# Kernel tuning notes

Hardware: AMD Instinct MI355X
Metric: run time of the kernel (lower is better)

The kernel has to match this reference:

```python
import jax, jax.numpy as jnp
import numpy as np

COST_CLASS, COST_BBOX, COST_GIOU = 1.0, 5.0, 2.0


def _cxcywh_to_xyxy(b):
    cx, cy, w, h = b[..., 0], b[..., 1], b[..., 2], b[..., 3]
    return jnp.stack([cx - 0.5 * w, cy - 0.5 * h, cx + 0.5 * w, cy + 0.5 * h], axis=-1)


def _generalized_box_iou(boxes1, boxes2):
    # boxes1 [N,4], boxes2 [M,4] in xyxy -> [N,M] GIoU
    area1 = (boxes1[:, 2] - boxes1[:, 0]) * (boxes1[:, 3] - boxes1[:, 1])
    area2 = (boxes2[:, 2] - boxes2[:, 0]) * (boxes2[:, 3] - boxes2[:, 1])
    lt = jnp.maximum(boxes1[:, None, :2], boxes2[None, :, :2])
    rb = jnp.minimum(boxes1[:, None, 2:], boxes2[None, :, 2:])
    wh = jnp.clip(rb - lt, 0.0)
    inter = wh[..., 0] * wh[..., 1]
    union = area1[:, None] + area2[None, :] - inter
    iou = inter / union
    lt_e = jnp.minimum(boxes1[:, None, :2], boxes2[None, :, :2])
    rb_e = jnp.maximum(boxes1[:, None, 2:], boxes2[None, :, 2:])
    wh_e = jnp.clip(rb_e - lt_e, 0.0)
    area_e = wh_e[..., 0] * wh_e[..., 1]
    return iou - (area_e - union) / area_e


def setup_inputs() -> dict:
    key = jax.random.key(0)
    k1, k2, k3, k4 = jax.random.split(key, 4)
    B, Q, NC, T = 16, 900, 92, 1600
    return {
        "class_logits": jax.random.normal(k1, (B, Q, NC), dtype=jnp.float32),
        "box_regression": jax.random.uniform(k2, (B, Q, 4), dtype=jnp.float32),
        "tgt_ids": jax.random.randint(k3, (T,), 0, NC, dtype=jnp.int64),
        "tgt_bbox": jax.random.uniform(k4, (T, 4), dtype=jnp.float32),
    }


def reference(class_logits, box_regression, tgt_ids, tgt_bbox):
    B, Q, NC = class_logits.shape
    out_prob = jax.nn.softmax(class_logits.reshape(B * Q, NC), axis=-1)  # [BQ, NC]
    out_bbox = box_regression.reshape(B * Q, 4)                          # [BQ, 4]
    cost_class = -out_prob[:, tgt_ids]                                   # [BQ, T]
    cost_bbox = jnp.sum(jnp.abs(out_bbox[:, None, :] - tgt_bbox[None, :, :]), axis=-1)  # L1 cdist
    cost_giou = -_generalized_box_iou(_cxcywh_to_xyxy(out_bbox), _cxcywh_to_xyxy(tgt_bbox))
    C = COST_BBOX * cost_bbox + COST_CLASS * cost_class + COST_GIOU * cost_giou
    return C.reshape(B, Q, -1)
```

## Files before the change

kernel.cpp:

```cpp
#include <hip/hip_runtime.h>
#include <math.h>

#define BB 16
#define QQ 900
#define NC 92
#define NCP 96
#define TT 1600
#define BQ (BB * QQ)

#define RT 2
#define RTILE 8
#define NK 25

__global__ __launch_bounds__(256)
void k_cost(const float* __restrict__ logits,
            const float* __restrict__ boxes,
            const int* __restrict__ tids,
            const float* __restrict__ tbox,
            float* __restrict__ out) {
    __shared__ float pexp[RTILE][NCP];

    const int row0 = blockIdx.x * RTILE;

    {
        int idx = threadIdx.x * 2;
        int r = idx / NCP, c = idx - r * NCP;
        float2 v = make_float2(0.0f, 0.0f);
        if (c < NC) {
            float2 lv = *(const float2*)&logits[(row0 + r) * NC + c];
            v.x = __expf(lv.x); v.y = __expf(lv.y);
        }
        *(float2*)&pexp[r][c] = v;
        if (threadIdx.x < 128) {
            int idx2 = 512 + threadIdx.x * 2;
            int r2 = idx2 / NCP, c2 = idx2 - r2 * NCP;
            float2 v2 = make_float2(0.0f, 0.0f);
            if (c2 < NC) {
                float2 lv = *(const float2*)&logits[(row0 + r2) * NC + c2];
                v2.x = __expf(lv.x); v2.y = __expf(lv.y);
            }
            *(float2*)&pexp[r2][c2] = v2;
        }
    }
    __syncthreads();

    {
        const int r  = threadIdx.x >> 5;
        const int ls = threadIdx.x & 31;
        float a = pexp[r][ls * 3];
        float b = pexp[r][ls * 3 + 1];
        float d = pexp[r][ls * 3 + 2];
        float s = a + b + d;
        s += __shfl_xor(s, 1);
        s += __shfl_xor(s, 2);
        s += __shfl_xor(s, 4);
        s += __shfl_xor(s, 8);
        s += __shfl_xor(s, 16);
        float rinv = __builtin_amdgcn_rcpf(s);
        pexp[r][ls * 3]     = a * rinv;
        pexp[r][ls * 3 + 1] = b * rinv;
        pexp[r][ls * 3 + 2] = d * rinv;
    }

    const int tl   = threadIdx.x & 63;
    const int rg   = threadIdx.x >> 6;
    const int rloc = rg * RT;
    const int rbase = row0 + rloc;

    float rcx[RT], rcy[RT], rw[RT], rh[RT];
    float rx0[RT], ry0[RT], rx1[RT], ry1[RT], rar[RT];
    #pragma unroll
    for (int j = 0; j < RT; ++j) {
        float4 bb = ((const float4*)boxes)[rbase + j];
        rcx[j] = bb.x; rcy[j] = bb.y; rw[j] = bb.z; rh[j] = bb.w;
        rx0[j] = bb.x - 0.5f * bb.z; ry0[j] = bb.y - 0.5f * bb.w;
        rx1[j] = bb.x + 0.5f * bb.z; ry1[j] = bb.y + 0.5f * bb.w;
        rar[j] = bb.z * bb.w;
    }
    __syncthreads();

    float* o0 = out + rbase * TT + tl;
    float4 tb = ((const float4*)tbox)[tl];
    int    id = tids[tl];
    #pragma unroll 5
    for (int k = 0; k < NK; ++k) {
        float4 tbn; int idn;
        if (k + 1 < NK) {
            tbn = ((const float4*)tbox)[(k + 1) * 64 + tl];
            idn = tids[(k + 1) * 64 + tl];
        }
        float tx0 = tb.x - 0.5f * tb.z, ty0 = tb.y - 0.5f * tb.w;
        float tx1 = tb.x + 0.5f * tb.z, ty1 = tb.y + 0.5f * tb.w;
        float tar = tb.z * tb.w;
        #pragma unroll
        for (int j = 0; j < RT; ++j) {
            float l1 = fabsf(rcx[j] - tb.x) + fabsf(rcy[j] - tb.y)
                     + fabsf(rw[j]  - tb.z) + fabsf(rh[j]  - tb.w);
            float iwu = fminf(rx1[j], tx1) - fmaxf(rx0[j], tx0);
            float ihu = fminf(ry1[j], ty1) - fmaxf(ry0[j], ty0);
            float inter = fmaxf(iwu, 0.0f) * fmaxf(ihu, 0.0f);
            float uni = rar[j] + tar - inter;
            float ew = (rw[j] + tb.z) - iwu;
            float eh = (rh[j] + tb.w) - ihu;
            float ea = ew * eh;
            float num = fmaf(ea, inter - uni, uni * uni);
            float rden = __builtin_amdgcn_rcpf(uni * ea);
            float p = pexp[rloc + j][id];
            float c = fmaf(5.0f, l1, -p);
            c = fmaf(-2.0f * num, rden, c);
            o0[j * TT + k * 64] = c;
        }
        tb = tbn; id = idn;
    }
}

extern "C" void kernel_launch(void* const* d_in, const int* in_sizes, int n_in,
                              void* d_out, int out_size, void* d_ws, size_t ws_size,
                              hipStream_t stream) {
    const float* logits = (const float*)d_in[0];
    const float* boxes  = (const float*)d_in[1];
    const int*   tids   = (const int*)  d_in[2];
    const float* tbox   = (const float*)d_in[3];
    float* out = (float*)d_out;

    k_cost<<<dim3(BQ / RTILE, 1), 256, 0, stream>>>(
        logits, boxes, tids, tbox, out);
}
```

Baseline: 28.14 us.

## Transpose softmax tile in LDS and process two targets per thread

The probability tile is stored class-major (pg[class][row], padded to 10) so each thread fetches the probabilities for both of its rows with a single float2 LDS read per target. Each thread now handles two adjacent targets per iteration, writing float2 stores to the output and loading target ids as int2. A tail block covers the last 64 targets. The goal is fewer LDS reads, wider global stores and fewer loop iterations. The cost is higher register pressure and the loss of the explicit prefetch of target data.

```diff
diff --git a/kernel.cpp b/kernel.cpp
--- a/kernel.cpp
+++ b/kernel.cpp
@@ -10,7 +10,7 @@
 
 #define RT 2
 #define RTILE 8
-#define NK 25
+#define NKP 12
 
 __global__ __launch_bounds__(256)
 void k_cost(const float* __restrict__ logits,
@@ -18,38 +18,26 @@
             const int* __restrict__ tids,
             const float* __restrict__ tbox,
             float* __restrict__ out) {
-    __shared__ float pexp[RTILE][NCP];
+    __shared__ float pg[NCP][10];
 
     const int row0 = blockIdx.x * RTILE;
 
-    {
-        int idx = threadIdx.x * 2;
+    #pragma unroll
+    for (int it = 0; it < 3; ++it) {
+        int idx = it * 256 + threadIdx.x;
         int r = idx / NCP, c = idx - r * NCP;
-        float2 v = make_float2(0.0f, 0.0f);
-        if (c < NC) {
-            float2 lv = *(const float2*)&logits[(row0 + r) * NC + c];
-            v.x = __expf(lv.x); v.y = __expf(lv.y);
-        }
-        *(float2*)&pexp[r][c] = v;
-        if (threadIdx.x < 128) {
-            int idx2 = 512 + threadIdx.x * 2;
-            int r2 = idx2 / NCP, c2 = idx2 - r2 * NCP;
-            float2 v2 = make_float2(0.0f, 0.0f);
-            if (c2 < NC) {
-                float2 lv = *(const float2*)&logits[(row0 + r2) * NC + c2];
-                v2.x = __expf(lv.x); v2.y = __expf(lv.y);
-            }
-            *(float2*)&pexp[r2][c2] = v2;
-        }
+        float v = 0.0f;
+        if (c < NC) v = __expf(logits[(row0 + r) * NC + c]);
+        pg[c][r] = v;
     }
     __syncthreads();
 
     {
         const int r  = threadIdx.x >> 5;
         const int ls = threadIdx.x & 31;
-        float a = pexp[r][ls * 3];
-        float b = pexp[r][ls * 3 + 1];
-        float d = pexp[r][ls * 3 + 2];
+        float a = pg[ls * 3][r];
+        float b = pg[ls * 3 + 1][r];
+        float d = pg[ls * 3 + 2][r];
         float s = a + b + d;
         s += __shfl_xor(s, 1);
         s += __shfl_xor(s, 2);
@@ -57,9 +45,9 @@
         s += __shfl_xor(s, 8);
         s += __shfl_xor(s, 16);
         float rinv = __builtin_amdgcn_rcpf(s);
-        pexp[r][ls * 3]     = a * rinv;
-        pexp[r][ls * 3 + 1] = b * rinv;
-        pexp[r][ls * 3 + 2] = d * rinv;
+        pg[ls * 3][r]     = a * rinv;
+        pg[ls * 3 + 1][r] = b * rinv;
+        pg[ls * 3 + 2][r] = d * rinv;
     }
 
     const int tl   = threadIdx.x & 63;
@@ -79,16 +67,69 @@
     }
     __syncthreads();
 
-    float* o0 = out + rbase * TT + tl;
-    float4 tb = ((const float4*)tbox)[tl];
-    int    id = tids[tl];
-    #pragma unroll 5
-    for (int k = 0; k < NK; ++k) {
-        float4 tbn; int idn;
-        if (k + 1 < NK) {
-            tbn = ((const float4*)tbox)[(k + 1) * 64 + tl];
-            idn = tids[(k + 1) * 64 + tl];
+    const float4* tb4 = (const float4*)tbox;
+    const int2*   id2 = (const int2*)tids;
+
+    #pragma unroll 4
+    for (int k = 0; k < NKP; ++k) {
+        const int tp = k * 64 + tl;
+        float4 ta = tb4[tp * 2];
+        float4 tc = tb4[tp * 2 + 1];
+        int2   ii = id2[tp];
+        float2 pa = *(const float2*)&pg[ii.x][rloc];
+        float2 pc = *(const float2*)&pg[ii.y][rloc];
+
+        float ax0 = ta.x - 0.5f * ta.z, ay0 = ta.y - 0.5f * ta.w;
+        float ax1 = ta.x + 0.5f * ta.z, ay1 = ta.y + 0.5f * ta.w;
+        float aar = ta.z * ta.w;
+        float cx0 = tc.x - 0.5f * tc.z, cy0 = tc.y - 0.5f * tc.w;
+        float cx1 = tc.x + 0.5f * tc.z, cy1 = tc.y + 0.5f * tc.w;
+        float car = tc.z * tc.w;
+
+        #pragma unroll
+        for (int j = 0; j < RT; ++j) {
+            float2 o;
+            {
+                float l1 = fabsf(rcx[j] - ta.x) + fabsf(rcy[j] - ta.y)
+                         + fabsf(rw[j]  - ta.z) + fabsf(rh[j]  - ta.w);
+                float iwu = fminf(rx1[j], ax1) - fmaxf(rx0[j], ax0);
+                float ihu = fminf(ry1[j], ay1) - fmaxf(ry0[j], ay0);
+                float inter = fmaxf(iwu, 0.0f) * fmaxf(ihu, 0.0f);
+                float uni = rar[j] + aar - inter;
+                float ew = (rw[j] + ta.z) - iwu;
+                float eh = (rh[j] + ta.w) - ihu;
+                float ea = ew * eh;
+                float num = fmaf(ea, inter - uni, uni * uni);
+                float rden = __builtin_amdgcn_rcpf(uni * ea);
+                float p = (j == 0) ? pa.x : pa.y;
+                float c = fmaf(5.0f, l1, -p);
+                o.x = fmaf(-2.0f * num, rden, c);
+            }
+            {
+                float l1 = fabsf(rcx[j] - tc.x) + fabsf(rcy[j] - tc.y)
+                         + fabsf(rw[j]  - tc.z) + fabsf(rh[j]  - tc.w);
+                float iwu = fminf(rx1[j], cx1) - fmaxf(rx0[j], cx0);
+                float ihu = fminf(ry1[j], cy1) - fmaxf(ry0[j], cy0);
+                float inter = fmaxf(iwu, 0.0f) * fmaxf(ihu, 0.0f);
+                float uni = rar[j] + car - inter;
+                float ew = (rw[j] + tc.z) - iwu;
+                float eh = (rh[j] + tc.w) - ihu;
+                float ea = ew * eh;
+                float num = fmaf(ea, inter - uni, uni * uni);
+                float rden = __builtin_amdgcn_rcpf(uni * ea);
+                float p = (j == 0) ? pc.x : pc.y;
+                float c = fmaf(5.0f, l1, -p);
+                o.y = fmaf(-2.0f * num, rden, c);
+            }
+            *(float2*)&out[(rbase + j) * TT + tp * 2] = o;
         }
+    }
+
+    {
+        const int t = NKP * 128 + tl;
+        float4 tb = tb4[t];
+        int    id = tids[t];
+        float2 pt = *(const float2*)&pg[id][rloc];
         float tx0 = tb.x - 0.5f * tb.z, ty0 = tb.y - 0.5f * tb.w;
         float tx1 = tb.x + 0.5f * tb.z, ty1 = tb.y + 0.5f * tb.w;
         float tar = tb.z * tb.w;
@@ -105,12 +146,11 @@
             float ea = ew * eh;
             float num = fmaf(ea, inter - uni, uni * uni);
             float rden = __builtin_amdgcn_rcpf(uni * ea);
-            float p = pexp[rloc + j][id];
+            float p = (j == 0) ? pt.x : pt.y;
             float c = fmaf(5.0f, l1, -p);
             c = fmaf(-2.0f * num, rden, c);
-            o0[j * TT + k * 64] = c;
+            out[(rbase + j) * TT + t] = c;
         }
-        tb = tbn; id = idn;
     }
 }
 
```

Result: slower. 33.95 us (+20.6%).
